# Performance work log

Hardware: AMD Instinct MI355X
Metric: run time of the kernel (lower is better)

## Reference

```python
import jax, jax.numpy as jnp
import numpy as np

B, L = 8, 512
EMB, NHEAD, HD = 512, 8, 64
FFN, NL = 2048, 6
VOCAB, NRE, RING_START, PAD, MAXLEN = 45, 20, 24, 0, 512
NOUT0 = VOCAB - NRE  # 25
NEG = -jnp.inf


def _ln(x, g, b, eps=1e-5):
    m = jnp.mean(x, -1, keepdims=True)
    v = jnp.mean((x - m) ** 2, -1, keepdims=True)
    return (x - m) * jax.lax.rsqrt(v + eps) * g + b


def setup_inputs():
    key = jax.random.key(0)
    ks = jax.random.split(key, 24)
    p = lambda k, shape: jax.random.normal(k, shape, jnp.float32) * 0.02
    return {
        "sequences": jax.random.randint(ks[0], (B, L), 1, VOCAB),  # avoid PAD=0
        "count_sequences": jax.random.randint(ks[1], (B, L), 0, MAXLEN),
        "graph_mask_sequences": jax.random.bernoulli(ks[2], 0.05, (B, L, VOCAB)),
        "valence_mask_sequences": jax.random.bernoulli(ks[3], 0.05, (B, L, VOCAB)),
        "linear_loc_squares": jax.random.randint(ks[4], (B, L, L), 0, MAXLEN + 1),
        "up_loc_squares": jax.random.randint(ks[5], (B, L, L), 0, MAXLEN + 1),
        "down_loc_squares": jax.random.randint(ks[6], (B, L, L), 0, MAXLEN + 1),
        "tok_emb": p(ks[7], (VOCAB, EMB)),
        "cnt_emb": p(ks[8], (MAXLEN, EMB)),
        "lin_loc_emb": p(ks[9], (MAXLEN + 1, NHEAD)),
        "up_loc_emb": p(ks[10], (MAXLEN + 1, NHEAD)),
        "down_loc_emb": p(ks[11], (MAXLEN + 1, NHEAD)),
        "in_proj_w": p(ks[12], (NL, 3 * EMB, EMB)),
        "in_proj_b": jnp.zeros((NL, 3 * EMB), jnp.float32),
        "out_w": p(ks[13], (NL, EMB, EMB)),
        "out_b": jnp.zeros((NL, EMB), jnp.float32),
        "ln1_g": jnp.ones((NL, EMB), jnp.float32),
        "ln1_b": jnp.zeros((NL, EMB), jnp.float32),
        "ln2_g": jnp.ones((NL, EMB), jnp.float32),
        "ln2_b": jnp.zeros((NL, EMB), jnp.float32),
        "ffn_w1": p(ks[14], (NL, FFN, EMB)),
        "ffn_b1": jnp.zeros((NL, FFN), jnp.float32),
        "ffn_w2": p(ks[15], (NL, EMB, FFN)),
        "ffn_b2": jnp.zeros((NL, EMB), jnp.float32),
        "fin_g": jnp.ones((EMB,), jnp.float32),
        "fin_b": jnp.zeros((EMB,), jnp.float32),
        "gen_w": p(ks[16], (NOUT0, EMB)),
        "gen_b": jnp.zeros((NOUT0,), jnp.float32),
        "ring_w0": p(ks[17], (EMB, EMB)),
        "ring_b0": jnp.zeros((EMB,), jnp.float32),
        "ring_w1": p(ks[18], (EMB, EMB)),
        "ring_b1": jnp.zeros((EMB,), jnp.float32),
    }


def _forward(tok_emb, cnt_emb, lin_loc_emb, up_loc_emb, down_loc_emb,
             in_proj_w, in_proj_b, out_w, out_b, ln1_g, ln1_b, ln2_g, ln2_b,
             ffn_w1, ffn_b1, ffn_w2, ffn_b2, fin_g, fin_b, gen_w, gen_b,
             ring_w0, ring_b0, ring_w1, ring_b1,
             sequences, count_sequences, graph_mask_sequences,
             valence_mask_sequences, linear_loc_squares, up_loc_squares,
             down_loc_squares):
    scale_e = jnp.sqrt(jnp.float32(EMB))
    x = tok_emb[sequences] * scale_e + cnt_emb[count_sequences] * scale_e  # (B,L,E)

    # per-head additive attention bias from three (B,L,L) index lookups
    bias = lin_loc_emb[linear_loc_squares] + up_loc_emb[up_loc_squares] + down_loc_emb[down_loc_squares]  # (B,L,L,H)
    bias = jnp.transpose(bias, (0, 3, 1, 2))  # (B,H,Lq,Lk)
    causal = jnp.tril(jnp.ones((L, L), bool))
    attn_bias = jnp.where(causal[None, None], bias, NEG)
    pad = sequences == PAD  # key padding
    attn_bias = jnp.where(pad[:, None, None, :], NEG, attn_bias)

    inv_sqrt_hd = 1.0 / jnp.sqrt(jnp.float32(HD))
    for i in range(NL):  # post-norm TransformerEncoderLayer, gelu
        qkv = jnp.einsum('ble,fe->blf', x, in_proj_w[i]) + in_proj_b[i]
        q, k, v = jnp.split(qkv, 3, axis=-1)
        q = q.reshape(B, L, NHEAD, HD)
        k = k.reshape(B, L, NHEAD, HD)
        v = v.reshape(B, L, NHEAD, HD)
        scores = jnp.einsum('bqhd,bkhd->bhqk', q, k) * inv_sqrt_hd + attn_bias
        a = jax.nn.softmax(scores, axis=-1)
        ctx = jnp.einsum('bhqk,bkhd->bqhd', a, v).reshape(B, L, EMB)
        attn_out = jnp.einsum('ble,fe->blf', ctx, out_w[i]) + out_b[i]
        x = _ln(x + attn_out, ln1_g[i], ln1_b[i])
        h = jax.nn.gelu(jnp.einsum('ble,fe->blf', x, ffn_w1[i]) + ffn_b1[i], approximate=False)
        ff = jnp.einsum('blf,ef->ble', h, ffn_w2[i]) + ffn_b2[i]
        x = _ln(x + ff, ln2_g[i], ln2_b[i])
    x = _ln(x, fin_g, fin_b)

    logits0 = jnp.einsum('ble,oe->blo', x, gen_w) + gen_b  # (B,L,NOUT0)

    # EdgeLogitLayer: scatter ring-start projections into NRE slots
    out0 = jnp.einsum('ble,he->blh', x, ring_w0) + ring_b0
    out1_ = jnp.einsum('ble,he->blh', x, ring_w1) + ring_b1
    ring_start = sequences == RING_START
    idx = jnp.where(ring_start, jnp.cumsum(ring_start.astype(jnp.int32), axis=1), 0)  # (B,L)
    bidx = jnp.arange(B)[:, None]
    slots = jnp.zeros((B, NRE + 1, EMB), x.dtype).at[bidx, idx].set(out1_, mode='drop')
    ring_tab = slots[:, 1:]  # drop slot 0 (non-ring-start writes)
    logits1 = jnp.einsum('ble,bre->blr', out0, ring_tab) * (EMB ** -0.5)

    logits = jnp.concatenate([logits0, logits1], axis=2)  # (B,L,VOCAB)
    logits = jnp.where(graph_mask_sequences, NEG, logits)
    logits = jnp.where(valence_mask_sequences, NEG, logits)
    return logits


def reference(sequences, count_sequences, graph_mask_sequences, valence_mask_sequences,
              linear_loc_squares, up_loc_squares, down_loc_squares,
              tok_emb, cnt_emb, lin_loc_emb, up_loc_emb, down_loc_emb,
              in_proj_w, in_proj_b, out_w, out_b, ln1_g, ln1_b, ln2_g, ln2_b,
              ffn_w1, ffn_b1, ffn_w2, ffn_b2, fin_g, fin_b, gen_w, gen_b,
              ring_w0, ring_b0, ring_w1, ring_b1):
    return _forward(tok_emb, cnt_emb, lin_loc_emb, up_loc_emb, down_loc_emb,
                    in_proj_w, in_proj_b, out_w, out_b, ln1_g, ln1_b, ln2_g, ln2_b,
                    ffn_w1, ffn_b1, ffn_w2, ffn_b2, fin_g, fin_b, gen_w, gen_b,
                    ring_w0, ring_b0, ring_w1, ring_b1,
                    sequences, count_sequences, graph_mask_sequences,
                    valence_mask_sequences, linear_loc_squares, up_loc_squares,
                    down_loc_squares)
```

## Files before the change

kernel.cpp:

```cpp
#include <hip/hip_runtime.h>
#include <cmath>

#define BB 8
#define LL 512
#define EMB 512
#define NHEAD 8
#define HD 64
#define FFN 2048
#define NL 6
#define VOCAB 45
#define NRE 20
#define RING_START 24
#define NOUT0 25
#define BL 4096

#define BIG_NEG -1.0e30f

typedef __bf16 bf16x8 __attribute__((ext_vector_type(8)));
typedef __bf16 bf16x4 __attribute__((ext_vector_type(4)));
typedef float f32x4 __attribute__((ext_vector_type(4)));

__device__ __forceinline__ void ld_g2l(const __bf16* g, __bf16* l) {
  __builtin_amdgcn_global_load_lds(
      (const __attribute__((address_space(1))) unsigned int*)g,
      (__attribute__((address_space(3))) unsigned int*)l, 16, 0, 0);
}

__global__ __launch_bounds__(256) void cast_kernel(
    const float* __restrict__ src, __bf16* __restrict__ dst, int n8) {
  const int gid = blockIdx.x * 256 + threadIdx.x;
  if (gid >= n8) return;
  const float4 a = ((const float4*)src)[gid * 2];
  const float4 b = ((const float4*)src)[gid * 2 + 1];
  bf16x8 v;
  v[0] = (__bf16)a.x; v[1] = (__bf16)a.y; v[2] = (__bf16)a.z; v[3] = (__bf16)a.w;
  v[4] = (__bf16)b.x; v[5] = (__bf16)b.y; v[6] = (__bf16)b.z; v[7] = (__bf16)b.w;
  *(bf16x8*)(dst + (size_t)gid * 8) = v;
}

__global__ __launch_bounds__(256) void concat2_kernel(
    const float* __restrict__ a, const float* __restrict__ b,
    float* __restrict__ o) {
  const int i = blockIdx.x * 256 + threadIdx.x;
  o[i] = (i < EMB) ? a[i] : b[i - EMB];
}

__global__ __launch_bounds__(128) void embed_kernel(
    const int* __restrict__ seq, const int* __restrict__ cnt,
    const float* __restrict__ tok_emb, const float* __restrict__ cnt_emb,
    float* __restrict__ x, __bf16* __restrict__ xb) {
  const int row = blockIdx.x;
  const int t = seq[row];
  const int c = cnt[row];
  const float scale = 22.627416997969522f;
  const int j = threadIdx.x * 4;
  float4 tv = *(const float4*)(tok_emb + (size_t)t * EMB + j);
  float4 cv = *(const float4*)(cnt_emb + (size_t)c * EMB + j);
  float4 o;
  o.x = (tv.x + cv.x) * scale;
  o.y = (tv.y + cv.y) * scale;
  o.z = (tv.z + cv.z) * scale;
  o.w = (tv.w + cv.w) * scale;
  *(float4*)(x + (size_t)row * EMB + j) = o;
  bf16x4 h;
  h[0] = (__bf16)o.x; h[1] = (__bf16)o.y; h[2] = (__bf16)o.z; h[3] = (__bf16)o.w;
  *(bf16x4*)(xb + (size_t)row * EMB + j) = h;
}

__global__ __launch_bounds__(256) void bias_kernel(
    const int* __restrict__ lin_sq, const int* __restrict__ up_sq,
    const int* __restrict__ down_sq,
    const __bf16* __restrict__ tl16, const __bf16* __restrict__ tu16,
    const __bf16* __restrict__ td16,
    const int* __restrict__ seq, __bf16* __restrict__ bias) {
  __shared__ __bf16 Tl[513 * 8], Tu[513 * 8], Td[513 * 8];
  __shared__ int seqs[LL];
  const int tid = threadIdx.x;
  const int b = blockIdx.x >> 6;
  const int q0 = (blockIdx.x & 63) * 8;
  for (int i = tid; i < 513; i += 256) {
    *(bf16x8*)&Tl[i * 8] = *(const bf16x8*)&tl16[i * 8];
    *(bf16x8*)&Tu[i * 8] = *(const bf16x8*)&tu16[i * 8];
    *(bf16x8*)&Td[i * 8] = *(const bf16x8*)&td16[i * 8];
  }
  for (int i = tid; i < LL; i += 256) seqs[i] = seq[b * LL + i];
  __syncthreads();
  for (int q = q0; q < q0 + 8; q++) {
    const size_t rbase = ((size_t)(b * LL + q)) * LL;
    for (int k = tid; k <= q; k += 256) {
      const int li = lin_sq[rbase + k], ui = up_sq[rbase + k],
                di = down_sq[rbase + k];
      const bool valid = (seqs[k] != 0);
      bf16x8 a = *(const bf16x8*)&Tl[li * 8];
      bf16x8 u = *(const bf16x8*)&Tu[ui * 8];
      bf16x8 d = *(const bf16x8*)&Td[di * 8];
#pragma unroll
      for (int h = 0; h < NHEAD; h++) {
        float v = valid ? ((float)a[h] + (float)u[h] + (float)d[h])
                        : -INFINITY;
        bias[(((size_t)(b * NHEAD + h) * LL) + q) * LL + k] = (__bf16)v;
      }
    }
  }
}

template <int BM, int BN, int ACT, int OUTBF, int RES, int SPLITK>
__global__ __launch_bounds__(256) void gemm_mfma_kernel(
    const __bf16* __restrict__ A, const __bf16* __restrict__ W,
    const float* __restrict__ bias, float* __restrict__ C,
    __bf16* __restrict__ Cb, const float* __restrict__ Res,
    int N, int K, int lda) {
  constexpr int MI = BM / 32;
  constexpr int NI = BN / 32;
  __shared__ __bf16 As[BM * 32];
  __shared__ __bf16 Ws[BN * 32];
  const int tid = threadIdx.x;
  const int lane = tid & 63, wave = tid >> 6;
  const int wm = wave >> 1, wn = wave & 1;
  const int q = lane >> 4, l15 = lane & 15;
  const int m0 = blockIdx.y * BM, n0 = blockIdx.x * BN;
  const int kz = SPLITK ? blockIdx.z : 0;

  const __bf16* Ag =
      A + (size_t)(m0 + (tid >> 2)) * lda + (tid & 3) * 8 + (size_t)kz * K;
  const __bf16* Wg =
      W + (size_t)(n0 + (tid >> 2)) * lda + (tid & 3) * 8 + (size_t)kz * K;
  __bf16* Al = &As[tid * 8];
  __bf16* Wl = &Ws[tid * 8];

  f32x4 acc[MI][NI] = {};

  for (int k0 = 0; k0 < K; k0 += 32) {
    ld_g2l(Ag + k0, Al);
    if (BM == 128) ld_g2l(Ag + k0 + (size_t)64 * lda, Al + 2048);
    ld_g2l(Wg + k0, Wl);
    if (BN == 128) ld_g2l(Wg + k0 + (size_t)64 * lda, Wl + 2048);
    __syncthreads();
    bf16x8 af[MI], bfr[NI];
#pragma unroll
    for (int mi = 0; mi < MI; mi++)
      af[mi] =
          *(const bf16x8*)&As[(wm * (BM / 2) + mi * 16 + l15) * 32 + q * 8];
#pragma unroll
    for (int ni = 0; ni < NI; ni++)
      bfr[ni] =
          *(const bf16x8*)&Ws[(wn * (BN / 2) + ni * 16 + l15) * 32 + q * 8];
#pragma unroll
    for (int mi = 0; mi < MI; mi++)
#pragma unroll
      for (int ni = 0; ni < NI; ni++)
        acc[mi][ni] = __builtin_amdgcn_mfma_f32_16x16x32_bf16(
            af[mi], bfr[ni], acc[mi][ni], 0, 0, 0);
    __syncthreads();
  }

  float* Cz = SPLITK ? (C + (size_t)kz * ((size_t)BL * N)) : C;
#pragma unroll
  for (int ni = 0; ni < NI; ni++) {
    const int n = n0 + wn * (BN / 2) + ni * 16 + l15;
    const float bv = (!SPLITK || kz == 0) ? bias[n] : 0.f;
#pragma unroll
    for (int mi = 0; mi < MI; mi++) {
#pragma unroll
      for (int r = 0; r < 4; r++) {
        const int m = m0 + wm * (BM / 2) + mi * 16 + q * 4 + r;
        float v = acc[mi][ni][r] + bv;
        if (RES && (!SPLITK || kz == 0)) v += Res[(size_t)m * N + n];
        if (ACT == 1) v = 0.5f * v * (1.0f + erff(v * 0.70710678118654752f));
        if (OUTBF)
          Cb[(size_t)m * N + n] = (__bf16)v;
        else
          Cz[(size_t)m * N + n] = v;
      }
    }
  }
}

__global__ __launch_bounds__(256) void attn_tile_kernel(
    const __bf16* __restrict__ qkv, const __bf16* __restrict__ bias,
    __bf16* __restrict__ Po, float2* __restrict__ Pml) {
  __shared__ __bf16 Qs[64][72];
  __shared__ __bf16 Ks[64][72];
  __shared__ __bf16 Vt[64][72];
  __shared__ __bf16 Ps[64][72];
  const int tid = threadIdx.x;
  const int lane = tid & 63, w = tid >> 6;
  const int q = lane >> 4, l15 = lane & 15;
  const int bh = blockIdx.y;
  const int b = bh >> 3, h = bh & 7;
  const int pidx = blockIdx.x;
  int qt = 0, acc0 = 0;
  while (acc0 + qt + 1 <= pidx) { acc0 += qt + 1; qt++; }
  const int kt = pidx - acc0;
  const int q0 = qt * 64, k0 = kt * 64;
  const bool diag = (qt == kt);
  const int slot = (bh * 8 + qt) * 8 + kt;
  const float inv_sqrt_hd = 0.125f;

  {
    const int row = tid >> 2, c0 = (tid & 3) * 16;
    const __bf16* qsrc = qkv + (size_t)(b * LL + q0 + row) * 1536 + h * HD + c0;
    *(bf16x8*)&Qs[row][c0] = *(const bf16x8*)qsrc;
    *(bf16x8*)&Qs[row][c0 + 8] = *(const bf16x8*)(qsrc + 8);
    const __bf16* src = qkv + (size_t)(b * LL + k0 + row) * 1536 + h * HD;
    bf16x8 kv0 = *(const bf16x8*)(src + 512 + c0);
    bf16x8 kv1 = *(const bf16x8*)(src + 512 + c0 + 8);
    bf16x8 vv0 = *(const bf16x8*)(src + 1024 + c0);
    bf16x8 vv1 = *(const bf16x8*)(src + 1024 + c0 + 8);
    *(bf16x8*)&Ks[row][c0] = kv0;
    *(bf16x8*)&Ks[row][c0 + 8] = kv1;
#pragma unroll
    for (int j = 0; j < 8; j++) {
      Vt[c0 + j][row] = vv0[j];
      Vt[c0 + 8 + j][row] = vv1[j];
    }
  }
  __syncthreads();

  f32x4 s4[4] = {};
  {
    bf16x8 aq0 = *(const bf16x8*)&Qs[w * 16 + l15][q * 8];
    bf16x8 aq1 = *(const bf16x8*)&Qs[w * 16 + l15][32 + q * 8];
#pragma unroll
    for (int ni = 0; ni < 4; ni++) {
      bf16x8 bk0 = *(const bf16x8*)&Ks[ni * 16 + l15][q * 8];
      bf16x8 bk1 = *(const bf16x8*)&Ks[ni * 16 + l15][32 + q * 8];
      s4[ni] = __builtin_amdgcn_mfma_f32_16x16x32_bf16(aq0, bk0, s4[ni], 0, 0, 0);
      s4[ni] = __builtin_amdgcn_mfma_f32_16x16x32_bf16(aq1, bk1, s4[ni], 0, 0, 0);
    }
  }

  const size_t bbase = ((size_t)bh * LL + (q0 + w * 16 + q * 4)) * LL + k0;
#pragma unroll
  for (int r = 0; r < 4; r++) {
    const int qrow = w * 16 + q * 4 + r;
    float sv[4];
#pragma unroll
    for (int ni = 0; ni < 4; ni++) {
      sv[ni] = s4[ni][r] * inv_sqrt_hd +
               (float)bias[bbase + (size_t)r * LL + ni * 16 + l15];
      if (diag && (ni * 16 + l15 > qrow)) sv[ni] = -INFINITY;
    }
    float tm = fmaxf(fmaxf(sv[0], sv[1]), fmaxf(sv[2], sv[3]));
#pragma unroll
    for (int off = 1; off < 16; off <<= 1)
      tm = fmaxf(tm, __shfl_xor(tm, off, 16));
    float rs = 0.f;
#pragma unroll
    for (int ni = 0; ni < 4; ni++) {
      const float p = expf(sv[ni] - tm);
      Ps[qrow][ni * 16 + l15] = (__bf16)p;
      rs += p;
    }
#pragma unroll
    for (int off = 1; off < 16; off <<= 1) rs += __shfl_xor(rs, off, 16);
    if (l15 == 0)
      Pml[(size_t)slot * 64 + qrow] = make_float2(tm, rs);
  }
  __syncthreads();

  f32x4 o4[4] = {};
  {
    bf16x8 ap0 = *(const bf16x8*)&Ps[w * 16 + l15][q * 8];
    bf16x8 ap1 = *(const bf16x8*)&Ps[w * 16 + l15][32 + q * 8];
#pragma unroll
    for (int ni = 0; ni < 4; ni++) {
      bf16x8 bv0 = *(const bf16x8*)&Vt[ni * 16 + l15][q * 8];
      bf16x8 bv1 = *(const bf16x8*)&Vt[ni * 16 + l15][32 + q * 8];
      o4[ni] = __builtin_amdgcn_mfma_f32_16x16x32_bf16(ap0, bv0, o4[ni], 0, 0, 0);
      o4[ni] = __builtin_amdgcn_mfma_f32_16x16x32_bf16(ap1, bv1, o4[ni], 0, 0, 0);
    }
  }
#pragma unroll
  for (int r = 0; r < 4; r++) {
    __bf16* dst = Po + (size_t)slot * 4096 + (w * 16 + q * 4 + r) * 64 + l15;
#pragma unroll
    for (int ni = 0; ni < 4; ni++) dst[ni * 16] = (__bf16)o4[ni][r];
  }
}

__global__ __launch_bounds__(256) void attn_combine_kernel(
    const __bf16* __restrict__ Po, const float2* __restrict__ Pml,
    __bf16* __restrict__ ctx) {
  const int tid = threadIdx.x;
  const int bh = blockIdx.x >> 3;
  const int qt = blockIdx.x & 7;
  const int b = bh >> 3, h = bh & 7;
  const int nkt = qt + 1;
  const int slot0 = (bh * 8 + qt) * 8;
  __shared__ float wls[8][64];
  __shared__ float invl[64];
  if (tid < 64) {
    float m = -3.0e38f;
    for (int kt = 0; kt < nkt; kt++)
      m = fmaxf(m, Pml[(size_t)(slot0 + kt) * 64 + tid].x);
    float l = 0.f;
    for (int kt = 0; kt < nkt; kt++) {
      const float2 ml = Pml[(size_t)(slot0 + kt) * 64 + tid];
      const float wk = expf(ml.x - m);
      wls[kt][tid] = wk;
      l += ml.y * wk;
    }
    invl[tid] = 1.0f / l;
  }
  __syncthreads();
  const int row = tid >> 2, d0 = (tid & 3) * 16;
  float acc[16] = {};
  for (int kt = 0; kt < nkt; kt++) {
    const __bf16* src = Po + (size_t)(slot0 + kt) * 4096 + row * 64 + d0;
    const float wk = wls[kt][row];
    bf16x8 v0 = *(const bf16x8*)src;
    bf16x8 v1 = *(const bf16x8*)(src + 8);
#pragma unroll
    for (int j = 0; j < 8; j++) {
      acc[j] += (float)v0[j] * wk;
      acc[8 + j] += (float)v1[j] * wk;
    }
  }
  const float il = invl[row];
  bf16x8 o0, o1;
#pragma unroll
  for (int j = 0; j < 8; j++) {
    o0[j] = (__bf16)(acc[j] * il);
    o1[j] = (__bf16)(acc[8 + j] * il);
  }
  __bf16* dst = ctx + (size_t)(b * LL + qt * 64 + row) * EMB + h * HD + d0;
  *(bf16x8*)dst = o0;
  *(bf16x8*)(dst + 8) = o1;
}

template <int NSUM>
__global__ __launch_bounds__(256) void add_ln_kernel(
    const float* __restrict__ xin, const float* __restrict__ g,
    const float* __restrict__ bta, float* __restrict__ out,
    __bf16* __restrict__ outb) {
  const int row = blockIdx.x;
  const int tid = threadIdx.x;
  float v0 = 0.f, v1 = 0.f;
#pragma unroll
  for (int sId = 0; sId < NSUM; sId++) {
    const float* xr = xin + (size_t)sId * BL * EMB + (size_t)row * EMB;
    v0 += xr[tid * 2];
    v1 += xr[tid * 2 + 1];
  }
  float s = v0 + v1, ss = v0 * v0 + v1 * v1;
#pragma unroll
  for (int off = 1; off < 64; off <<= 1) {
    s += __shfl_xor(s, off, 64);
    ss += __shfl_xor(ss, off, 64);
  }
  __shared__ float sbuf[8];
  const int wave = tid >> 6, lane = tid & 63;
  if (lane == 0) { sbuf[wave] = s; sbuf[4 + wave] = ss; }
  __syncthreads();
  s = sbuf[0] + sbuf[1] + sbuf[2] + sbuf[3];
  ss = sbuf[4] + sbuf[5] + sbuf[6] + sbuf[7];
  const float mean = s * (1.0f / EMB);
  const float var = ss * (1.0f / EMB) - mean * mean;
  const float rstd = rsqrtf(var + 1e-5f);
  const float o0 = (v0 - mean) * rstd * g[tid * 2] + bta[tid * 2];
  const float o1 = (v1 - mean) * rstd * g[tid * 2 + 1] + bta[tid * 2 + 1];
  float* orow = out + (size_t)row * EMB;
  orow[tid * 2] = o0;
  orow[tid * 2 + 1] = o1;
  if (outb) {
    __bf16* brow = outb + (size_t)row * EMB;
    brow[tid * 2] = (__bf16)o0;
    brow[tid * 2 + 1] = (__bf16)o1;
  }
}

__global__ __launch_bounds__(256) void ring_scatter_kernel(
    const int* __restrict__ seq, const float* __restrict__ o01,
    float* __restrict__ ring_tab) {
  const int b = blockIdx.x;
  const int tid = threadIdx.x;
  float* rt = ring_tab + (size_t)b * NRE * EMB;
  for (int i = tid; i < NRE * EMB; i += 256) rt[i] = 0.f;
  __shared__ int pos[NRE];
  __shared__ int cntr;
  if (tid == 0) {
    int c = 0;
    for (int l = 0; l < LL; l++) {
      if (seq[b * LL + l] == RING_START) {
        c++;
        if (c <= NRE) pos[c - 1] = l;
      }
    }
    cntr = (c < NRE) ? c : NRE;
  }
  __syncthreads();
  const int n = cntr;
  for (int r = 0; r < n; r++) {
    const float* src = o01 + (size_t)(b * LL + pos[r]) * 1024 + 512;
    for (int i = tid; i < EMB; i += 256) rt[r * EMB + i] = src[i];
  }
}

__global__ __launch_bounds__(256) void head_kernel(
    const float* __restrict__ xf, const float* __restrict__ o01,
    const float* __restrict__ ring_tab, const float* __restrict__ gen_w,
    const float* __restrict__ gen_b, const int* __restrict__ gmask,
    const int* __restrict__ vmask, float* __restrict__ out) {
  const int row = blockIdx.x;
  const int b = row >> 9;
  const int tid = threadIdx.x;
  __shared__ float xr[EMB], o0s[EMB];
  {
    float2 a = ((const float2*)(xf + (size_t)row * EMB))[tid];
    ((float2*)xr)[tid] = a;
    float2 c = ((const float2*)(o01 + (size_t)row * 1024))[tid];
    ((float2*)o0s)[tid] = c;
  }
  __syncthreads();
  const int wave = tid >> 6, lane = tid & 63;
  for (int o = wave; o < VOCAB; o += 4) {
    const float* wrow;
    const float* src;
    float bv, scale;
    if (o < NOUT0) {
      wrow = gen_w + (size_t)o * EMB;
      bv = gen_b[o];
      src = xr;
      scale = 1.0f;
    } else {
      wrow = ring_tab + ((size_t)b * NRE + (o - NOUT0)) * EMB;
      bv = 0.0f;
      src = o0s;
      scale = 0.044194173824159216f;
    }
    float sum = 0.f;
#pragma unroll
    for (int j = 0; j < 8; j++) {
      const int d = lane + 64 * j;
      sum += src[d] * wrow[d];
    }
#pragma unroll
    for (int off = 1; off < 64; off <<= 1) sum += __shfl_xor(sum, off, 64);
    if (lane == 0) {
      float v = sum * scale + bv;
      const size_t oidx = (size_t)row * VOCAB + o;
      if (gmask[oidx] != 0 || vmask[oidx] != 0) v = BIG_NEG;
      out[oidx] = v;
    }
  }
}

extern "C" void kernel_launch(void* const* d_in, const int* in_sizes, int n_in,
                              void* d_out, int out_size, void* d_ws,
                              size_t ws_size, hipStream_t stream) {
  const int* seq = (const int*)d_in[0];
  const int* cnt = (const int*)d_in[1];
  const int* gmask = (const int*)d_in[2];
  const int* vmask = (const int*)d_in[3];
  const int* lin_sq = (const int*)d_in[4];
  const int* up_sq = (const int*)d_in[5];
  const int* down_sq = (const int*)d_in[6];
  const float* tok_emb = (const float*)d_in[7];
  const float* cnt_emb = (const float*)d_in[8];
  const float* lin_e = (const float*)d_in[9];
  const float* up_e = (const float*)d_in[10];
  const float* down_e = (const float*)d_in[11];
  const float* in_proj_w = (const float*)d_in[12];
  const float* in_proj_b = (const float*)d_in[13];
  const float* out_w = (const float*)d_in[14];
  const float* out_b = (const float*)d_in[15];
  const float* ln1_g = (const float*)d_in[16];
  const float* ln1_b = (const float*)d_in[17];
  const float* ln2_g = (const float*)d_in[18];
  const float* ln2_b = (const float*)d_in[19];
  const float* ffn_w1 = (const float*)d_in[20];
  const float* ffn_b1 = (const float*)d_in[21];
  const float* ffn_w2 = (const float*)d_in[22];
  const float* ffn_b2 = (const float*)d_in[23];
  const float* fin_g = (const float*)d_in[24];
  const float* fin_b = (const float*)d_in[25];
  const float* gen_w = (const float*)d_in[26];
  const float* gen_b = (const float*)d_in[27];
  const float* ring_w0 = (const float*)d_in[28];
  const float* ring_b0 = (const float*)d_in[29];
  const float* ring_w1 = (const float*)d_in[30];
  const float* ring_b1 = (const float*)d_in[31];

  char* p = (char*)d_ws;
  auto alloc_f = [&](size_t n) { float* r = (float*)p; p += n * 4; return r; };
  auto alloc_h = [&](size_t n) { __bf16* r = (__bf16*)p; p += n * 2; return r; };

  float* x = alloc_f((size_t)BL * EMB);
  float* pbuf = alloc_f((size_t)2 * BL * EMB);
  float* xfb = alloc_f((size_t)BL * EMB);
  float* o01b = alloc_f((size_t)BL * 1024);
  float* ringb = alloc_f((size_t)BB * NRE * EMB);
  float* biasr = alloc_f(1024);
  float2* attn_pml = (float2*)alloc_f((size_t)4096 * 64 * 2);
  __bf16* attn_po = alloc_h((size_t)4096 * 4096);
  __bf16* biasb = alloc_h((size_t)BB * NHEAD * LL * LL);
  __bf16* xb = alloc_h((size_t)BL * EMB);
  __bf16* qkvb16 = alloc_h((size_t)BL * 3 * EMB);
  __bf16* ctxb = alloc_h((size_t)BL * EMB);
  __bf16* hb = alloc_h((size_t)BL * FFN);
  __bf16* xfb16 = alloc_h((size_t)BL * EMB);
  __bf16* wqkv = alloc_h((size_t)NL * 3 * EMB * EMB);
  __bf16* wout = alloc_h((size_t)NL * EMB * EMB);
  __bf16* wf1 = alloc_h((size_t)NL * FFN * EMB);
  __bf16* wf2 = alloc_h((size_t)NL * EMB * FFN);
  __bf16* wr01 = alloc_h((size_t)2 * EMB * EMB);
  __bf16* tl16 = hb;
  __bf16* tu16 = hb + 4104;
  __bf16* td16 = hb + 8208;

  auto cast = [&](const float* s, __bf16* d, size_t n) {
    const int n8 = (int)(n / 8);
    cast_kernel<<<(n8 + 255) / 256, 256, 0, stream>>>(s, d, n8);
  };
  cast(in_proj_w, wqkv, (size_t)NL * 3 * EMB * EMB);
  cast(out_w, wout, (size_t)NL * EMB * EMB);
  cast(ffn_w1, wf1, (size_t)NL * FFN * EMB);
  cast(ffn_w2, wf2, (size_t)NL * EMB * FFN);
  cast(ring_w0, wr01, (size_t)EMB * EMB);
  cast(ring_w1, wr01 + (size_t)EMB * EMB, (size_t)EMB * EMB);
  cast(lin_e, tl16, (size_t)513 * 8);
  cast(up_e, tu16, (size_t)513 * 8);
  cast(down_e, td16, (size_t)513 * 8);
  concat2_kernel<<<4, 256, 0, stream>>>(ring_b0, ring_b1, biasr);

  embed_kernel<<<BL, 128, 0, stream>>>(seq, cnt, tok_emb, cnt_emb, x, xb);
  bias_kernel<<<BB * 64, 256, 0, stream>>>(lin_sq, up_sq, down_sq, tl16, tu16,
                                           td16, seq, biasb);

  for (int i = 0; i < NL; i++) {
    gemm_mfma_kernel<64, 128, 0, 1, 0, 0><<<dim3(12, 64), 256, 0, stream>>>(
        xb, wqkv + (size_t)i * 3 * EMB * EMB, in_proj_b + (size_t)i * 3 * EMB,
        nullptr, qkvb16, nullptr, 3 * EMB, EMB, EMB);
    attn_tile_kernel<<<dim3(36, 64), 256, 0, stream>>>(qkvb16, biasb, attn_po,
                                                       attn_pml);
    attn_combine_kernel<<<512, 256, 0, stream>>>(attn_po, attn_pml, ctxb);
    gemm_mfma_kernel<64, 64, 0, 0, 1, 1><<<dim3(8, 64, 2), 256, 0, stream>>>(
        ctxb, wout + (size_t)i * EMB * EMB, out_b + (size_t)i * EMB, pbuf,
        nullptr, x, EMB, EMB / 2, EMB);
    add_ln_kernel<2><<<BL, 256, 0, stream>>>(
        pbuf, ln1_g + (size_t)i * EMB, ln1_b + (size_t)i * EMB, x, xb);
    gemm_mfma_kernel<64, 128, 1, 1, 0, 0><<<dim3(16, 64), 256, 0, stream>>>(
        xb, wf1 + (size_t)i * FFN * EMB, ffn_b1 + (size_t)i * FFN, nullptr, hb,
        nullptr, FFN, EMB, EMB);
    gemm_mfma_kernel<64, 64, 0, 0, 1, 1><<<dim3(8, 64, 2), 256, 0, stream>>>(
        hb, wf2 + (size_t)i * EMB * FFN, ffn_b2 + (size_t)i * EMB, pbuf,
        nullptr, x, EMB, FFN / 2, FFN);
    add_ln_kernel<2><<<BL, 256, 0, stream>>>(
        pbuf, ln2_g + (size_t)i * EMB, ln2_b + (size_t)i * EMB, x, xb);
  }

  add_ln_kernel<1><<<BL, 256, 0, stream>>>(x, fin_g, fin_b, xfb, xfb16);
  gemm_mfma_kernel<64, 128, 0, 0, 0, 0><<<dim3(8, 64), 256, 0, stream>>>(
      xfb16, wr01, biasr, o01b, nullptr, nullptr, 1024, EMB, EMB);
  ring_scatter_kernel<<<BB, 256, 0, stream>>>(seq, o01b, ringb);
  head_kernel<<<BL, 256, 0, stream>>>(xfb, o01b, ringb, gen_w, gen_b, gmask,
                                      vmask, (float*)d_out);
}
```

Measured before the change: 1.054 ms.

## Fuse output and FFN2 projections with residual add and LayerNorm

Replaces the split-K out-projection and FFN2 GEMMs plus the separate add+LayerNorm kernels with one kernel. Each block computes a full 16-row by 512-column output tile, adds bias and residual, reduces row statistics across waves in shared memory and writes the normalized fp32 and bf16 activations. This drops the partial-sum buffer round trip and two launches per layer. The cost is only 256 blocks with narrow M tiles, so each block reloads the whole weight tile per 16 rows, which lowers weight reuse and occupancy. Residual is read from and written to the same buffer in place.

```diff
diff --git a/kernel.cpp b/kernel.cpp
--- a/kernel.cpp
+++ b/kernel.cpp
@@ -104,12 +104,11 @@
   }
 }
 
-template <int BM, int BN, int ACT, int OUTBF, int RES, int SPLITK>
+template <int BM, int BN, int ACT, int OUTBF>
 __global__ __launch_bounds__(256) void gemm_mfma_kernel(
     const __bf16* __restrict__ A, const __bf16* __restrict__ W,
     const float* __restrict__ bias, float* __restrict__ C,
-    __bf16* __restrict__ Cb, const float* __restrict__ Res,
-    int N, int K, int lda) {
+    __bf16* __restrict__ Cb, int N, int K) {
   constexpr int MI = BM / 32;
   constexpr int NI = BN / 32;
   __shared__ __bf16 As[BM * 32];
@@ -119,12 +118,9 @@
   const int wm = wave >> 1, wn = wave & 1;
   const int q = lane >> 4, l15 = lane & 15;
   const int m0 = blockIdx.y * BM, n0 = blockIdx.x * BN;
-  const int kz = SPLITK ? blockIdx.z : 0;
-
-  const __bf16* Ag =
-      A + (size_t)(m0 + (tid >> 2)) * lda + (tid & 3) * 8 + (size_t)kz * K;
-  const __bf16* Wg =
-      W + (size_t)(n0 + (tid >> 2)) * lda + (tid & 3) * 8 + (size_t)kz * K;
+
+  const __bf16* Ag = A + (size_t)(m0 + (tid >> 2)) * K + (tid & 3) * 8;
+  const __bf16* Wg = W + (size_t)(n0 + (tid >> 2)) * K + (tid & 3) * 8;
   __bf16* Al = &As[tid * 8];
   __bf16* Wl = &Ws[tid * 8];
 
@@ -132,9 +128,9 @@
 
   for (int k0 = 0; k0 < K; k0 += 32) {
     ld_g2l(Ag + k0, Al);
-    if (BM == 128) ld_g2l(Ag + k0 + (size_t)64 * lda, Al + 2048);
+    if (BM == 128) ld_g2l(Ag + k0 + (size_t)64 * K, Al + 2048);
     ld_g2l(Wg + k0, Wl);
-    if (BN == 128) ld_g2l(Wg + k0 + (size_t)64 * lda, Wl + 2048);
+    if (BN == 128) ld_g2l(Wg + k0 + (size_t)64 * K, Wl + 2048);
     __syncthreads();
     bf16x8 af[MI], bfr[NI];
 #pragma unroll
@@ -154,24 +150,116 @@
     __syncthreads();
   }
 
-  float* Cz = SPLITK ? (C + (size_t)kz * ((size_t)BL * N)) : C;
 #pragma unroll
   for (int ni = 0; ni < NI; ni++) {
     const int n = n0 + wn * (BN / 2) + ni * 16 + l15;
-    const float bv = (!SPLITK || kz == 0) ? bias[n] : 0.f;
+    const float bv = bias[n];
 #pragma unroll
     for (int mi = 0; mi < MI; mi++) {
 #pragma unroll
       for (int r = 0; r < 4; r++) {
         const int m = m0 + wm * (BM / 2) + mi * 16 + q * 4 + r;
         float v = acc[mi][ni][r] + bv;
-        if (RES && (!SPLITK || kz == 0)) v += Res[(size_t)m * N + n];
         if (ACT == 1) v = 0.5f * v * (1.0f + erff(v * 0.70710678118654752f));
         if (OUTBF)
           Cb[(size_t)m * N + n] = (__bf16)v;
         else
-          Cz[(size_t)m * N + n] = v;
+          C[(size_t)m * N + n] = v;
       }
+    }
+  }
+}
+
+template <int RES>
+__global__ __launch_bounds__(256) void gemm_ln_kernel(
+    const __bf16* __restrict__ A, const __bf16* __restrict__ W,
+    const float* __restrict__ bias, const float* __restrict__ Res,
+    const float* __restrict__ g, const float* __restrict__ bta,
+    float* __restrict__ outx, __bf16* __restrict__ outxb, int K) {
+  __shared__ __bf16 As[16 * 32];
+  __shared__ __bf16 Ws[512 * 32];
+  __shared__ float lnS[4][16], lnQ[4][16];
+  const int tid = threadIdx.x;
+  const int lane = tid & 63, w = tid >> 6;
+  const int q = lane >> 4, l15 = lane & 15;
+  const int m0 = blockIdx.x * 16;
+
+  const __bf16* Ag = A + (size_t)(m0 + (lane >> 2)) * K + (lane & 3) * 8;
+  f32x4 acc[8] = {};
+
+  for (int k0 = 0; k0 < K; k0 += 32) {
+    if (w == 0) ld_g2l(Ag + k0, &As[lane * 8]);
+#pragma unroll
+    for (int j = 0; j < 8; j++) {
+      const int rowbase = w * 128 + j * 16;
+      ld_g2l(W + (size_t)(rowbase + (lane >> 2)) * K + (lane & 3) * 8 + k0,
+             &Ws[rowbase * 32 + lane * 8]);
+    }
+    __syncthreads();
+    bf16x8 af = *(const bf16x8*)&As[l15 * 32 + q * 8];
+#pragma unroll
+    for (int ni = 0; ni < 8; ni++) {
+      bf16x8 bfr =
+          *(const bf16x8*)&Ws[(w * 128 + ni * 16 + l15) * 32 + q * 8];
+      acc[ni] =
+          __builtin_amdgcn_mfma_f32_16x16x32_bf16(af, bfr, acc[ni], 0, 0, 0);
+    }
+    __syncthreads();
+  }
+
+  const int col0 = w * 128;
+  float v[8][4];
+  float ps[4] = {}, pq[4] = {};
+#pragma unroll
+  for (int ni = 0; ni < 8; ni++) {
+    const int n = col0 + ni * 16 + l15;
+    const float bv = bias[n];
+#pragma unroll
+    for (int r = 0; r < 4; r++) {
+      const int m = m0 + q * 4 + r;
+      float t = acc[ni][r] + bv;
+      if (RES) t += Res[(size_t)m * EMB + n];
+      v[ni][r] = t;
+      ps[r] += t;
+      pq[r] += t * t;
+    }
+  }
+#pragma unroll
+  for (int r = 0; r < 4; r++) {
+#pragma unroll
+    for (int off = 1; off < 16; off <<= 1) {
+      ps[r] += __shfl_xor(ps[r], off, 16);
+      pq[r] += __shfl_xor(pq[r], off, 16);
+    }
+  }
+  if (l15 == 0) {
+#pragma unroll
+    for (int r = 0; r < 4; r++) {
+      lnS[w][q * 4 + r] = ps[r];
+      lnQ[w][q * 4 + r] = pq[r];
+    }
+  }
+  __syncthreads();
+  float mean[4], rstd[4];
+#pragma unroll
+  for (int r = 0; r < 4; r++) {
+    const int row = q * 4 + r;
+    const float S = lnS[0][row] + lnS[1][row] + lnS[2][row] + lnS[3][row];
+    const float Q = lnQ[0][row] + lnQ[1][row] + lnQ[2][row] + lnQ[3][row];
+    mean[r] = S * (1.0f / EMB);
+    const float var = Q * (1.0f / EMB) - mean[r] * mean[r];
+    rstd[r] = rsqrtf(var + 1e-5f);
+  }
+#pragma unroll
+  for (int ni = 0; ni < 8; ni++) {
+    const int n = col0 + ni * 16 + l15;
+    const float gv = g[n], bv = bta[n];
+#pragma unroll
+    for (int r = 0; r < 4; r++) {
+      const int m = m0 + q * 4 + r;
+      const float o = (v[ni][r] - mean[r]) * rstd[r] * gv + bv;
+      outx[(size_t)m * EMB + n] = o;
+      outxb[(size_t)m * EMB + n] = (__bf16)o;
     }
   }
 }
@@ -329,20 +417,14 @@
   *(bf16x8*)(dst + 8) = o1;
 }
 
-template <int NSUM>
 __global__ __launch_bounds__(256) void add_ln_kernel(
     const float* __restrict__ xin, const float* __restrict__ g,
     const float* __restrict__ bta, float* __restrict__ out,
     __bf16* __restrict__ outb) {
   const int row = blockIdx.x;
   const int tid = threadIdx.x;
-  float v0 = 0.f, v1 = 0.f;
-#pragma unroll
-  for (int sId = 0; sId < NSUM; sId++) {
-    const float* xr = xin + (size_t)sId * BL * EMB + (size_t)row * EMB;
-    v0 += xr[tid * 2];
-    v1 += xr[tid * 2 + 1];
-  }
+  const float* xr = xin + (size_t)row * EMB;
+  float v0 = xr[tid * 2], v1 = xr[tid * 2 + 1];
   float s = v0 + v1, ss = v0 * v0 + v1 * v1;
 #pragma unroll
   for (int off = 1; off < 64; off <<= 1) {
@@ -487,7 +569,6 @@
   auto alloc_h = [&](size_t n) { __bf16* r = (__bf16*)p; p += n * 2; return r; };
 
   float* x = alloc_f((size_t)BL * EMB);
-  float* pbuf = alloc_f((size_t)2 * BL * EMB);
   float* xfb = alloc_f((size_t)BL * EMB);
   float* o01b = alloc_f((size_t)BL * 1024);
   float* ringb = alloc_f((size_t)BB * NRE * EMB);
@@ -529,30 +610,26 @@
                                            td16, seq, biasb);
 
   for (int i = 0; i < NL; i++) {
-    gemm_mfma_kernel<64, 128, 0, 1, 0, 0><<<dim3(12, 64), 256, 0, stream>>>(
+    gemm_mfma_kernel<64, 128, 0, 1><<<dim3(12, 64), 256, 0, stream>>>(
         xb, wqkv + (size_t)i * 3 * EMB * EMB, in_proj_b + (size_t)i * 3 * EMB,
-        nullptr, qkvb16, nullptr, 3 * EMB, EMB, EMB);
+        nullptr, qkvb16, 3 * EMB, EMB);
     attn_tile_kernel<<<dim3(36, 64), 256, 0, stream>>>(qkvb16, biasb, attn_po,
                                                        attn_pml);
     attn_combine_kernel<<<512, 256, 0, stream>>>(attn_po, attn_pml, ctxb);
-    gemm_mfma_kernel<64, 64, 0, 0, 1, 1><<<dim3(8, 64, 2), 256, 0, stream>>>(
-        ctxb, wout + (size_t)i * EMB * EMB, out_b + (size_t)i * EMB, pbuf,
-        nullptr, x, EMB, EMB / 2, EMB);
-    add_ln_kernel<2><<<BL, 256, 0, stream>>>(
-        pbuf, ln1_g + (size_t)i * EMB, ln1_b + (size_t)i * EMB, x, xb);
-    gemm_mfma_kernel<64, 128, 1, 1, 0, 0><<<dim3(16, 64), 256, 0, stream>>>(
+    gemm_ln_kernel<1><<<256, 256, 0, stream>>>(
+        ctxb, wout + (size_t)i * EMB * EMB, out_b + (size_t)i * EMB, x,
+        ln1_g + (size_t)i * EMB, ln1_b + (size_t)i * EMB, x, xb, EMB);
+    gemm_mfma_kernel<64, 128, 1, 1><<<dim3(16, 64), 256, 0, stream>>>(
         xb, wf1 + (size_t)i * FFN * EMB, ffn_b1 + (size_t)i * FFN, nullptr, hb,
-        nullptr, FFN, EMB, EMB);
-    gemm_mfma_kernel<64, 64, 0, 0, 1, 1><<<dim3(8, 64, 2), 256, 0, stream>>>(
-        hb, wf2 + (size_t)i * EMB * FFN, ffn_b2 + (size_t)i * EMB, pbuf,
-        nullptr, x, EMB, FFN / 2, FFN);
-    add_ln_kernel<2><<<BL, 256, 0, stream>>>(
-        pbuf, ln2_g + (size_t)i * EMB, ln2_b + (size_t)i * EMB, x, xb);
-  }
-
-  add_ln_kernel<1><<<BL, 256, 0, stream>>>(x, fin_g, fin_b, xfb, xfb16);
-  gemm_mfma_kernel<64, 128, 0, 0, 0, 0><<<dim3(8, 64), 256, 0, stream>>>(
-      xfb16, wr01, biasr, o01b, nullptr, nullptr, 1024, EMB, EMB);
+        FFN, EMB);
+    gemm_ln_kernel<1><<<256, 256, 0, stream>>>(
+        hb, wf2 + (size_t)i * EMB * FFN, ffn_b2 + (size_t)i * EMB, x,
+        ln2_g + (size_t)i * EMB, ln2_b + (size_t)i * EMB, x, xb, FFN);
+  }
+
+  add_ln_kernel<<<BL, 256, 0, stream>>>(x, fin_g, fin_b, xfb, xfb16);
+  gemm_mfma_kernel<64, 128, 0, 0><<<dim3(8, 64), 256, 0, stream>>>(
+      xfb16, wr01, biasr, o01b, nullptr, 1024, EMB);
   ring_scatter_kernel<<<BB, 256, 0, stream>>>(seq, o01b, ringb);
   head_kernel<<<BL, 256, 0, stream>>>(xfb, o01b, ringb, gen_w, gen_b, gmask,
                                       vmask, (float*)d_out);
```

Measured after the change: 1.215 ms. 1.15x slower.
